# Performance work log

Measured on AMD Instinct MI355X. Metric: run time of the kernel, lower is better.

Reference implementation:

```python
import jax, jax.numpy as jnp
import numpy as np
import math

EPS = 1e-6
MAX_NORM = 1.0 - 1e-3


def _clip_to_ball(x):
    # Keep point strictly inside the unit ball (||x|| < 1).
    norm = jnp.maximum(jnp.linalg.norm(x, axis=-1, keepdims=True), EPS)
    factor = jnp.minimum(MAX_NORM / norm, 1.0)
    return x * factor


def setup_inputs() -> dict:
    key = jax.random.key(0)
    k1, k2 = jax.random.split(key)
    B, C, D = 8192, 4096, 512
    euclidean_emb = jax.random.normal(k1, (B, D), dtype=jnp.float32)
    centroids = jax.random.uniform(k2, (C, D), dtype=jnp.float32, minval=-0.01, maxval=0.01)
    log_c = jnp.asarray(math.log(1.0), dtype=jnp.float32)
    return {"euclidean_emb": euclidean_emb, "log_c": log_c, "centroids": centroids}


def reference(euclidean_emb, log_c, centroids):
    # torch code used c = self.log_c.exp().item() -> c is detached scalar
    c = jax.lax.stop_gradient(jnp.exp(log_c))
    sqrt_c = jnp.sqrt(c)

    # expmap0: Euclidean -> Poincare ball
    v_norm = jnp.maximum(jnp.linalg.norm(euclidean_emb, axis=-1, keepdims=True), EPS)
    coeff = jnp.tanh(sqrt_c * v_norm) / (sqrt_c * v_norm)
    x_h = _clip_to_ball(coeff * euclidean_emb)   # (B, D)
    cen_h = _clip_to_ball(centroids)             # (C, D)

    # Pairwise Poincare distance via GEMM (same math as the expanded (B,C,D) form):
    # ||x - y||^2 = ||x||^2 + ||y||^2 - 2 <x, y>
    x2_raw = jnp.sum(x_h * x_h, axis=-1)         # (B,)
    y2_raw = jnp.sum(cen_h * cen_h, axis=-1)     # (C,)
    x2 = jnp.minimum(x2_raw, MAX_NORM ** 2)
    y2 = jnp.minimum(y2_raw, MAX_NORM ** 2)
    xy = x_h @ cen_h.T                           # (B, C) GEMM
    diff2 = x2_raw[:, None] + y2_raw[None, :] - 2.0 * xy

    denom = jnp.maximum((1.0 - c * x2)[:, None] * (1.0 - c * y2)[None, :], EPS)
    arg = jnp.maximum(1.0 + c * (2.0 * diff2) / denom, 1.0 + EPS)
    dists = jnp.arccosh(arg) / sqrt_c            # (B, C)
    return dists, x_h, cen_h
```

## Files before the change

### kernel.cpp

```cpp
#include <hip/hip_runtime.h>
#include <math.h>

#define EPSV 1e-6f
#define MAX_NORM (1.0f - 1e-3f)

typedef __attribute__((ext_vector_type(8))) short short8;
typedef __attribute__((ext_vector_type(4))) float f32x4;

__device__ inline ushort f32_to_bf16(float f) {
    union { float f; uint32_t u; } cv;
    cv.f = f;
    uint32_t u = cv.u;
    u += 0x7FFFu + ((u >> 16) & 1u);
    return (ushort)(u >> 16);
}

__device__ inline void glds16(const ushort* gsrc, ushort* ldsdst) {
    auto* g = (const __attribute__((address_space(1))) uint32_t*)gsrc;
    auto* l = (__attribute__((address_space(3))) uint32_t*)ldsdst;
    __builtin_amdgcn_global_load_lds(g, l, 16, 0, 0);
}

__global__ void rows_emb_kernel(const float* __restrict__ emb,
                                const float* __restrict__ logc,
                                float* __restrict__ xh,
                                ushort* __restrict__ xbf,
                                float* __restrict__ x2raw,
                                float* __restrict__ dxv) {
    const int D = 512;
    const int row = blockIdx.x;
    const int lane = threadIdx.x;

    const float4* r4 = (const float4*)(emb + (size_t)row * D);
    float4 a = r4[2 * lane];
    float4 b = r4[2 * lane + 1];

    float ss = a.x * a.x + a.y * a.y + a.z * a.z + a.w * a.w
             + b.x * b.x + b.y * b.y + b.z * b.z + b.w * b.w;
#pragma unroll
    for (int off = 32; off > 0; off >>= 1) ss += __shfl_xor(ss, off, 64);

    const float c  = expf(logc[0]);
    const float sc = sqrtf(c);

    const float tn    = sqrtf(ss);
    const float vn    = fmaxf(tn, EPSV);
    const float coeff = tanhf(sc * vn) / (sc * vn);
    const float pre   = coeff * tn;
    const float fac   = fminf(MAX_NORM / fmaxf(pre, EPSV), 1.0f);
    const float scale = coeff * fac;

    float4 oa, ob;
    oa.x = a.x * scale; oa.y = a.y * scale; oa.z = a.z * scale; oa.w = a.w * scale;
    ob.x = b.x * scale; ob.y = b.y * scale; ob.z = b.z * scale; ob.w = b.w * scale;

    float4* o4 = (float4*)(xh + (size_t)row * D);
    o4[2 * lane]     = oa;
    o4[2 * lane + 1] = ob;

    union { ushort u[8]; uint4 v; } pk;
    pk.u[0] = f32_to_bf16(oa.x); pk.u[1] = f32_to_bf16(oa.y);
    pk.u[2] = f32_to_bf16(oa.z); pk.u[3] = f32_to_bf16(oa.w);
    pk.u[4] = f32_to_bf16(ob.x); pk.u[5] = f32_to_bf16(ob.y);
    pk.u[6] = f32_to_bf16(ob.z); pk.u[7] = f32_to_bf16(ob.w);
    ((uint4*)(xbf + (size_t)row * D))[lane] = pk.v;

    if (lane == 0) {
        const float sq = scale * scale * ss;
        x2raw[row] = sq;
        dxv[row]   = 1.0f - c * fminf(sq, MAX_NORM * MAX_NORM);
    }
}

__global__ void rows_cen_kernel(const float* __restrict__ cen,
                                const float* __restrict__ logc,
                                float* __restrict__ ch,
                                ushort* __restrict__ cbf,
                                float* __restrict__ y2raw,
                                float* __restrict__ dyv) {
    const int D = 512;
    const int row = blockIdx.x;
    const int lane = threadIdx.x;

    const float4* r4 = (const float4*)(cen + (size_t)row * D);
    float4 a = r4[2 * lane];
    float4 b = r4[2 * lane + 1];

    float ss = a.x * a.x + a.y * a.y + a.z * a.z + a.w * a.w
             + b.x * b.x + b.y * b.y + b.z * b.z + b.w * b.w;
#pragma unroll
    for (int off = 32; off > 0; off >>= 1) ss += __shfl_xor(ss, off, 64);

    const float c = expf(logc[0]);

    const float tn    = sqrtf(ss);
    const float scale = fminf(MAX_NORM / fmaxf(tn, EPSV), 1.0f);

    float4 oa, ob;
    oa.x = a.x * scale; oa.y = a.y * scale; oa.z = a.z * scale; oa.w = a.w * scale;
    ob.x = b.x * scale; ob.y = b.y * scale; ob.z = b.z * scale; ob.w = b.w * scale;

    float4* o4 = (float4*)(ch + (size_t)row * D);
    o4[2 * lane]     = oa;
    o4[2 * lane + 1] = ob;

    union { ushort u[8]; uint4 v; } pk;
    pk.u[0] = f32_to_bf16(oa.x); pk.u[1] = f32_to_bf16(oa.y);
    pk.u[2] = f32_to_bf16(oa.z); pk.u[3] = f32_to_bf16(oa.w);
    pk.u[4] = f32_to_bf16(ob.x); pk.u[5] = f32_to_bf16(ob.y);
    pk.u[6] = f32_to_bf16(ob.z); pk.u[7] = f32_to_bf16(ob.w);
    ((uint4*)(cbf + (size_t)row * D))[lane] = pk.v;

    if (lane == 0) {
        const float sq = scale * scale * ss;
        y2raw[row] = sq;
        dyv[row]   = 1.0f - c * fminf(sq, MAX_NORM * MAX_NORM);
    }
}

#define BM 256
#define BN 256
#define BKT 64
#define EPST 68

__global__ __launch_bounds__(512, 2)
void gemm_epi_kernel(const ushort* __restrict__ Abf,
                     const ushort* __restrict__ Bbf,
                     const float* __restrict__ x2raw,
                     const float* __restrict__ dxv,
                     const float* __restrict__ y2raw,
                     const float* __restrict__ dyv,
                     const float* __restrict__ logc,
                     float* __restrict__ out,
                     int M, int N, int K) {
    __shared__ __align__(16) ushort As[2][32 * 512];
    __shared__ __align__(16) ushort Bs[2][32 * 512];

    const int tid  = threadIdx.x;
    const int lane = tid & 63;
    const int wid  = tid >> 6;
    const int wm   = wid >> 2;
    const int wn   = wid & 3;

    const int bm = blockIdx.y;
    const int bn = blockIdx.x;

    const ushort* Ab = Abf + (size_t)bm * BM * K;
    const ushort* Bb = Bbf + (size_t)bn * BN * K;

    f32x4 acc[8][4];
#pragma unroll
    for (int m = 0; m < 8; m++)
#pragma unroll
        for (int n = 0; n < 4; n++) acc[m][n] = (f32x4){0.f, 0.f, 0.f, 0.f};

    const size_t fragoff = (size_t)(lane & 15) * K + ((lane >> 4) * 8);

    auto stage = [&](int p, int k0) {
#pragma unroll
        for (int j = 0; j < 4; j++) {
            const int s  = wid * 4 + j;
            const int rg = s >> 1;
            const int kk = s & 1;
            const size_t goff = (size_t)(rg * 16) * K + k0 + kk * 32 + fragoff;
            glds16(Ab + goff, &As[p][s * 512]);
            glds16(Bb + goff, &Bs[p][s * 512]);
        }
    };

    stage(0, 0);
    __syncthreads();

    const int NT = K / BKT;
    int p = 0;
    for (int t = 0; t < NT; t++) {
        if (t + 1 < NT) stage(p ^ 1, (t + 1) * BKT);

#pragma unroll
        for (int kk = 0; kk < 2; kk++) {
            short8 af[8], bfr[4];
#pragma unroll
            for (int m = 0; m < 8; m++)
                af[m] = *(const short8*)(&As[p][((wm * 8 + m) * 2 + kk) * 512 + lane * 8]);
#pragma unroll
            for (int n = 0; n < 4; n++)
                bfr[n] = *(const short8*)(&Bs[p][((wn * 4 + n) * 2 + kk) * 512 + lane * 8]);
#pragma unroll
            for (int m = 0; m < 8; m++)
#pragma unroll
                for (int n = 0; n < 4; n++)
                    acc[m][n] = __builtin_amdgcn_mfma_f32_16x16x32_bf16(
                        af[m], bfr[n], acc[m][n], 0, 0, 0);
        }

        if (t + 1 < NT) __syncthreads();
        p ^= 1;
    }

    __syncthreads();

    const float c   = expf(logc[0]);
    const float rsc = 1.0f / sqrtf(c);
    const int l16 = lane & 15;
    const int lg  = lane >> 4;

    float* ep = (float*)((char*)As + (size_t)wid * 4352);
    const int gr_base = bm * BM + wm * 128;
    const int gc_base = bn * BN + wn * 64;

#pragma unroll
    for (int m = 0; m < 8; m++) {
#pragma unroll
        for (int n = 0; n < 4; n++)
#pragma unroll
            for (int r = 0; r < 4; r++)
                ep[(lg * 4 + r) * EPST + n * 16 + l16] = acc[m][n][r];
        asm volatile("s_waitcnt lgkmcnt(0)" ::: "memory");

#pragma unroll
        for (int it = 0; it < 4; it++) {
            const int row = it * 4 + lg;
            const int gr  = gr_base + m * 16 + row;
            const int gc  = gc_base + l16 * 4;
            float4 xy4 = *(const float4*)&ep[row * EPST + l16 * 4];
            const float rx  = x2raw[gr];
            const float dxr = dxv[gr];
            const float4 ry4 = *(const float4*)&y2raw[gc];
            const float4 dy4 = *(const float4*)&dyv[gc];
            float4 o;
            {
                const float rden = __builtin_amdgcn_rcpf(fmaxf(dxr * dy4.x, EPSV));
                float t = fmaxf(2.0f * c * (rx + ry4.x - 2.0f * xy4.x) * rden, EPSV);
                o.x = __logf(1.0f + t + __builtin_amdgcn_sqrtf(t * (t + 2.0f))) * rsc;
            }
            {
                const float rden = __builtin_amdgcn_rcpf(fmaxf(dxr * dy4.y, EPSV));
                float t = fmaxf(2.0f * c * (rx + ry4.y - 2.0f * xy4.y) * rden, EPSV);
                o.y = __logf(1.0f + t + __builtin_amdgcn_sqrtf(t * (t + 2.0f))) * rsc;
            }
            {
                const float rden = __builtin_amdgcn_rcpf(fmaxf(dxr * dy4.z, EPSV));
                float t = fmaxf(2.0f * c * (rx + ry4.z - 2.0f * xy4.z) * rden, EPSV);
                o.z = __logf(1.0f + t + __builtin_amdgcn_sqrtf(t * (t + 2.0f))) * rsc;
            }
            {
                const float rden = __builtin_amdgcn_rcpf(fmaxf(dxr * dy4.w, EPSV));
                float t = fmaxf(2.0f * c * (rx + ry4.w - 2.0f * xy4.w) * rden, EPSV);
                o.w = __logf(1.0f + t + __builtin_amdgcn_sqrtf(t * (t + 2.0f))) * rsc;
            }
            *(float4*)&out[(size_t)gr * N + gc] = o;
        }
        asm volatile("s_waitcnt lgkmcnt(0)" ::: "memory");
    }
}

extern "C" void kernel_launch(void* const* d_in, const int* in_sizes, int n_in,
                              void* d_out, int out_size, void* d_ws, size_t ws_size,
                              hipStream_t stream) {
    const float* emb  = (const float*)d_in[0];
    const float* logc = (const float*)d_in[1];
    const float* cen  = (const float*)d_in[2];

    const int D = 512;
    const int B = in_sizes[0] / D;
    const int C = in_sizes[2] / D;

    float* out   = (float*)d_out;
    float* dists = out;
    float* xh    = out + (size_t)B * C;
    float* ch    = xh + (size_t)B * D;

    char* ws = (char*)d_ws;
    size_t off = 0;
    auto alloc = [&](size_t bytes) -> char* {
        char* p = ws + off;
        off += (bytes + 255) & ~(size_t)255;
        return p;
    };
    ushort* xbf   = (ushort*)alloc((size_t)B * D * sizeof(ushort));
    ushort* cbf   = (ushort*)alloc((size_t)C * D * sizeof(ushort));
    float*  x2raw = (float*)alloc((size_t)B * sizeof(float));
    float*  dxv   = (float*)alloc((size_t)B * sizeof(float));
    float*  y2raw = (float*)alloc((size_t)C * sizeof(float));
    float*  dyv   = (float*)alloc((size_t)C * sizeof(float));

    rows_emb_kernel<<<B, 64, 0, stream>>>(emb, logc, xh, xbf, x2raw, dxv);
    rows_cen_kernel<<<C, 64, 0, stream>>>(cen, logc, ch, cbf, y2raw, dyv);

    dim3 grid(C / BN, B / BM);
    gemm_epi_kernel<<<grid, 512, 0, stream>>>(xbf, cbf, x2raw, dxv, y2raw, dyv,
                                              logc, dists, B, C, D);
}
```

Measured before the change: 99.92 us.

## Prefetch two K-tiles ahead with fine-grained vmcnt waits and MFMA priority

Restructures the GEMM main loop so two LDS buffers are kept in flight. The next tile's global-to-LDS loads are issued right after the current compute, and the code waits only on older loads using explicit vmcnt counters rather than full __syncthreads. LDS fragment reads become inline-asm ds_read_b128 followed by an lgkmcnt wait, and a sched_barrier plus s_setprio raise wave priority during the MFMA burst. The aim is to hide global load latency and reduce barrier stalls. The hand-written waitcnt values depend on the exact load count per stage, so a miscount would break correctness, and the asm LDS reads may prevent the compiler from interleaving them with other instructions.

```diff
diff --git a/kernel.cpp b/kernel.cpp
--- a/kernel.cpp
+++ b/kernel.cpp
@@ -19,6 +19,14 @@
     auto* g = (const __attribute__((address_space(1))) uint32_t*)gsrc;
     auto* l = (__attribute__((address_space(3))) uint32_t*)ldsdst;
     __builtin_amdgcn_global_load_lds(g, l, 16, 0, 0);
+}
+
+__device__ inline short8 ds_read128(const ushort* p) {
+    auto* l3 = (const __attribute__((address_space(3))) ushort*)p;
+    const uint32_t addr = (uint32_t)(uintptr_t)l3;
+    short8 v;
+    asm volatile("ds_read_b128 %0, %1" : "=&v"(v) : "v"(addr));
+    return v;
 }
 
 __global__ void rows_emb_kernel(const float* __restrict__ emb,
@@ -169,31 +177,44 @@
     };
 
     stage(0, 0);
-    __syncthreads();
+    stage(1, BKT);
+    asm volatile("s_waitcnt vmcnt(8)" ::: "memory");
+    __builtin_amdgcn_s_barrier();
 
     const int NT = K / BKT;
     int p = 0;
     for (int t = 0; t < NT; t++) {
-        if (t + 1 < NT) stage(p ^ 1, (t + 1) * BKT);
-
 #pragma unroll
         for (int kk = 0; kk < 2; kk++) {
             short8 af[8], bfr[4];
 #pragma unroll
             for (int m = 0; m < 8; m++)
-                af[m] = *(const short8*)(&As[p][((wm * 8 + m) * 2 + kk) * 512 + lane * 8]);
+                af[m] = ds_read128(&As[p][((wm * 8 + m) * 2 + kk) * 512 + lane * 8]);
 #pragma unroll
             for (int n = 0; n < 4; n++)
-                bfr[n] = *(const short8*)(&Bs[p][((wn * 4 + n) * 2 + kk) * 512 + lane * 8]);
+                bfr[n] = ds_read128(&Bs[p][((wn * 4 + n) * 2 + kk) * 512 + lane * 8]);
+            asm volatile("s_waitcnt lgkmcnt(0)" ::: "memory");
+            __builtin_amdgcn_sched_barrier(0);
+            __builtin_amdgcn_s_setprio(1);
 #pragma unroll
             for (int m = 0; m < 8; m++)
 #pragma unroll
                 for (int n = 0; n < 4; n++)
                     acc[m][n] = __builtin_amdgcn_mfma_f32_16x16x32_bf16(
                         af[m], bfr[n], acc[m][n], 0, 0, 0);
+            __builtin_amdgcn_s_setprio(0);
         }
 
-        if (t + 1 < NT) __syncthreads();
+        __builtin_amdgcn_s_barrier();
+
+        if (t + 2 < NT) {
+            stage(p, (t + 2) * BKT);
+            asm volatile("s_waitcnt vmcnt(8)" ::: "memory");
+            __builtin_amdgcn_s_barrier();
+        } else if (t + 1 < NT) {
+            asm volatile("s_waitcnt vmcnt(0)" ::: "memory");
+            __builtin_amdgcn_s_barrier();
+        }
         p ^= 1;
     }
 
```

Result: faster. 93.57 us (-6.4%).
